# Kernel tuning notes

Hardware: AMD Instinct MI355X
Metric: run time of the kernel (lower is better)

## Reference

```python
import jax, jax.numpy as jnp
import numpy as np

V = 27578   # super-model vertex count (self.shape)
NJ = 24     # joints
NB = 10     # shape PCA coeffs
NP = (NJ - 1) * 9  # 207 pose-blend features
K = 24000   # kept vertices (to_keep)
B = 32
# standard SMPL kinematic tree: PARENTS[i] is the parent joint of joint i (i>=1)
PARENTS = np.array([0, 0, 0, 0, 1, 2, 3, 4, 5, 6, 7, 8, 9, 9, 9, 12, 13, 14, 16, 17, 18, 19, 20, 21], dtype=np.int32)


def setup_inputs() -> dict:
    key = jax.random.key(0)
    ks = jax.random.split(key, 8)
    pose = jax.random.normal(ks[0], (B, NJ, 3), dtype=jnp.float32) * 0.4
    betas = jax.random.normal(ks[1], (B, NB + 1), dtype=jnp.float32)  # last entry = gender flag
    J_regressor = jax.random.uniform(ks[2], (2, NJ, V), dtype=jnp.float32)
    J_regressor = J_regressor / jnp.sum(J_regressor, axis=-1, keepdims=True)
    v_template = jax.random.normal(ks[3], (2, V, 3), dtype=jnp.float32)
    shapedirs = jax.random.normal(ks[4], (2, V, 3, NB), dtype=jnp.float32) * 0.03
    posedirs = jax.random.normal(ks[5], (2, V, 3, NP), dtype=jnp.float32) * 0.01
    weights_all = jax.random.uniform(ks[6], (2, V, NJ), dtype=jnp.float32)
    weights_all = weights_all / jnp.sum(weights_all, axis=-1, keepdims=True)
    to_keep = jnp.sort(jax.random.randint(ks[7], (K,), 0, V, dtype=jnp.int32))
    return {"pose": pose, "betas": betas, "J_regressor": J_regressor,
            "v_template": v_template, "shapedirs": shapedirs, "posedirs": posedirs,
            "weights_all": weights_all, "to_keep": to_keep}


def rodrigues(r):
    """Axis-angle [N,3] -> rotation matrices [N,3,3] (Rodrigues formula)."""
    eps = jnp.float32(np.finfo(np.float32).eps)
    theta = jnp.maximum(jnp.linalg.norm(r, axis=-1, keepdims=True), eps)  # [N,1]
    rh = r / theta
    z = jnp.zeros_like(rh[:, 0])
    m = jnp.stack([z, -rh[:, 2], rh[:, 1],
                   rh[:, 2], z, -rh[:, 0],
                   -rh[:, 1], rh[:, 0], z], axis=1).reshape(-1, 3, 3)
    t = theta[:, :, None]  # [N,1,1]
    I = jnp.eye(3, dtype=r.dtype)
    return I + m * jnp.sin(t) + jnp.matmul(m, m) * (1.0 - jnp.cos(t))


def reference(pose, betas, J_regressor, v_template, shapedirs, posedirs, weights_all, to_keep):
    b = betas.shape[0]
    dt = pose.dtype
    g = betas[:, -1] > 0.5  # gender: True -> male (index 1)
    sel = lambda f, m: jnp.where(g[:, None, None], m, f)

    # shape blendshapes for both genders, select per sample
    vs_f = jnp.einsum('bs,vcs->bvc', betas[:, :NB], shapedirs[0]) + v_template[0]
    vs_m = jnp.einsum('bs,vcs->bvc', betas[:, :NB], shapedirs[1]) + v_template[1]

    J_f = jnp.einsum('jv,bvc->bjc', J_regressor[0], vs_f)
    J_m = jnp.einsum('jv,bvc->bjc', J_regressor[1], vs_m)
    J = sel(J_f, J_m)  # [b,24,3]

    # Rodrigues per joint
    R = rodrigues(pose.reshape(-1, 3)).reshape(b, NJ, 3, 3)

    # pose blendshapes
    lrot = (R[:, 1:] - jnp.eye(3, dtype=dt)).reshape(b, NP)  # [b,207]
    off_f = jnp.einsum('bp,vcp->bvc', lrot, posedirs[0])
    off_m = jnp.einsum('bp,vcp->bvc', lrot, posedirs[1])
    v_posed = sel(vs_f, vs_m) + sel(off_f, off_m)  # [b,V,3]

    # local joint transforms [b,24,4,4]
    J_rel = jnp.concatenate([J[:, :1], J[:, 1:] - J[:, PARENTS[1:]]], axis=1)
    A = jnp.concatenate([R, J_rel[..., None]], axis=-1)  # [b,24,3,4]
    bottom = jnp.broadcast_to(jnp.array([0., 0., 0., 1.], dtype=dt), (b, NJ, 1, 4))
    A = jnp.concatenate([A, bottom], axis=2)

    # kinematic chain (sequential 24-joint tree)
    Gs = [A[:, 0]]
    for i in range(1, NJ):
        Gs.append(jnp.matmul(Gs[int(PARENTS[i])], A[:, i]))
    G = jnp.stack(Gs, axis=1)  # [b,24,4,4]

    # subtract rest-pose joint contribution: results = G - pack(G @ [J;0])
    Jh0 = jnp.concatenate([J, jnp.zeros((b, NJ, 1), dtype=dt)], axis=-1)
    corr = jnp.einsum('bjpq,bjq->bjp', G, Jh0)
    results = G.at[:, :, :, 3].add(-corr)

    Jh1 = jnp.concatenate([J, jnp.ones((b, NJ, 1), dtype=dt)], axis=-1)
    joints = jnp.einsum('bjpq,bjq->bjp', results, Jh1)[:, :, :3]

    # linear blend skinning with gender-matched weights
    w = jnp.where(g[:, None, None], weights_all[1][None], weights_all[0][None])  # [b,V,24]
    T = jnp.einsum('bjpq,bvj->bvpq', results, w)  # [b,V,4,4]
    vh = jnp.concatenate([v_posed, jnp.ones((b, V, 1), dtype=dt)], axis=-1)
    v = jnp.einsum('bvpq,bvq->bvp', T, vh)[:, :, :3]

    root = joints[:, :1]
    result = (v - root)[:, to_keep, :]  # [b,K,3]
    return result
```

## Files before the change

### kernel.cpp

```cpp
#include <hip/hip_runtime.h>
#include <hip/hip_bf16.h>
#include <cstdint>
#include <cstddef>

#define V      27578
#define NJ     24
#define KK     24000
#define NT2    1724
#define NCHUNK 21
#define VCHUNK 1314

#define LPD    0
#define LA     12288
#define LRB    16000
#define LVP    24192
#define LT     26368
#define LWA    36608
#define LTM2   37120
#define LROOT2 37216
#define LPERM2 37312
#define LCNT2  37344
#define LKB    37348
#define LDSW   37364

#define WS_JS   0
#define WS_LA   33264
#define WS_RB   36976
#define WS_ROOT 45168
#define WS_PERM 45264
#define WS_CNT  45296
#define WS_KB   45300

typedef short short8 __attribute__((ext_vector_type(8)));
typedef float f32x4 __attribute__((ext_vector_type(4)));
typedef float f32x4a __attribute__((ext_vector_type(4), aligned(4)));

union S8U4 { unsigned u[4]; uint4 u4; short8 s; };

__device__ __forceinline__ unsigned pk2(float a, float b) {
    __hip_bfloat162 h = __float22bfloat162_rn(float2{a, b});
    union { __hip_bfloat162 h; unsigned u; } cv; cv.h = h;
    return cv.u;
}

#define BAR_LGKM() do { \
    asm volatile("s_waitcnt lgkmcnt(0)\n\ts_barrier" ::: "memory"); \
    __builtin_amdgcn_sched_barrier(0); \
} while (0)

__constant__ int d_par[24] = {0,0,0,0,1,2,3,4,5,6,7,8,9,9,9,12,13,14,16,17,18,19,20,21};

__global__ __launch_bounds__(256) void k_js(const float* __restrict__ jreg,
                                            const float* __restrict__ vtmpl,
                                            const float* __restrict__ sdirs,
                                            float* __restrict__ ws) {
    const int chunk = blockIdx.x, jg = blockIdx.y, g = blockIdx.z;
    const int tid = threadIdx.x;
    float acc[4][33];
#pragma unroll
    for (int a = 0; a < 4; ++a)
#pragma unroll
        for (int o = 0; o < 33; ++o) acc[a][o] = 0.f;

    const int v0 = chunk * VCHUNK;
    const int v1 = (v0 + VCHUNK < V) ? v0 + VCHUNK : V;
    const float* jr0 = jreg + (size_t)g * NJ * V;
    const float* sd  = sdirs + (size_t)g * V * 30;
    const float* tm  = vtmpl + (size_t)g * V * 3;

    for (int v = v0 + tid; v < v1; v += 256) {
        float jv[4];
#pragma unroll
        for (int a = 0; a < 4; ++a) jv[a] = jr0[(size_t)(jg*4 + a) * V + v];
        float b[33];
        const float* sdv = sd + (size_t)v * 30;
#pragma unroll
        for (int o = 0; o < 30; o += 2) {
            float2 q = *(const float2*)(sdv + o);
            b[o] = q.x; b[o+1] = q.y;
        }
        b[30] = tm[(size_t)v*3 + 0];
        b[31] = tm[(size_t)v*3 + 1];
        b[32] = tm[(size_t)v*3 + 2];
#pragma unroll
        for (int a = 0; a < 4; ++a)
#pragma unroll
            for (int o = 0; o < 33; ++o) acc[a][o] += jv[a] * b[o];
    }

#pragma unroll
    for (int a = 0; a < 4; ++a)
#pragma unroll
        for (int o = 0; o < 33; ++o) {
            float x = acc[a][o];
#pragma unroll
            for (int s = 32; s >= 1; s >>= 1) x += __shfl_xor(x, s, 64);
            acc[a][o] = x;
        }

    __shared__ float red[4][132];
    const int wvi = tid >> 6, ln = tid & 63;
    if (ln == 0) {
#pragma unroll
        for (int a = 0; a < 4; ++a)
#pragma unroll
            for (int o = 0; o < 33; ++o) red[wvi][a*33 + o] = acc[a][o];
    }
    __syncthreads();
    if (tid < 132) {
        float s = red[0][tid] + red[1][tid] + red[2][tid] + red[3][tid];
        int a = tid / 33, o = tid % 33;
        int j = jg * 4 + a;
        ws[(size_t)((g*NJ + j)*33 + o) * NCHUNK + chunk] = s;
    }
}

__global__ __launch_bounds__(256) void k_joint(const float* __restrict__ pose,
                                               const float* __restrict__ betas,
                                               const int*   __restrict__ to_keep,
                                               float* __restrict__ ws) {
    const int bid = (int)blockIdx.x;
    const int t = threadIdx.x;
    int* wsI = (int*)ws;
    unsigned* wsU = (unsigned*)ws;

    if (bid >= 32) {
        int idx = (bid - 32) * 256 + t;
        if (idx <= NT2) {
            int target = idx * 16;
            int lo = 0, hi = KK;
            while (lo < hi) { int m = (lo + hi) >> 1; if (to_keep[m] < target) lo = m + 1; else hi = m; }
            wsI[WS_KB + idx] = lo;
        }
        return;
    }

    __shared__ float gflag[32];
    __shared__ int   permJ[33];
    __shared__ float jsJ[792];
    __shared__ float Jloc[96];
    __shared__ float AJ[288];
    __shared__ float GS[288];

    if (t < 32) gflag[t] = betas[t*11 + 10];
    __syncthreads();
    if (t < 32) {
        bool male = gflag[t] > 0.5f;
        unsigned gm = (unsigned)__ballot(male);
        int cnt0 = 32 - __popc(gm);
        unsigned below = (1u << t) - 1u;
        int slot = male ? (cnt0 + __popc(gm & below)) : __popc((~gm) & below);
        permJ[slot] = t;
        if (t == 0) permJ[32] = cnt0;
    }
    __syncthreads();

    const int slot = bid;
    const int b = permJ[slot];
    const int gi = (gflag[b] > 0.5f) ? 1 : 0;

    if (bid == 0) {
        if (t < 32) wsI[WS_PERM + t] = permJ[t];
        if (t == 0) wsI[WS_CNT] = permJ[32];
    }

    for (int o = t; o < 792; o += 256) {
        const float* p = ws + WS_JS + (size_t)(gi*792 + o) * NCHUNK;
        float s = 0.f;
#pragma unroll
        for (int c = 0; c < NCHUNK; ++c) s += p[c];
        jsJ[o] = s;
    }
    __syncthreads();

    if (t < 72) {
        int j = t / 3, c = t - 3*j;
        const float* jsb = jsJ + j*33;
        float s = jsb[30 + c];
#pragma unroll
        for (int q = 0; q < 10; ++q) s += jsb[c*10 + q] * betas[b*11 + q];
        Jloc[j*4 + c] = s;
    }
    __syncthreads();

    if (t < 24) {
        const float* pp = pose + (size_t)(b*24 + t) * 3;
        float rx = pp[0], ry = pp[1], rz = pp[2];
        float th = fmaxf(sqrtf(rx*rx + ry*ry + rz*rz), 1.1920929e-07f);
        float inv = 1.0f / th;
        float ux = rx*inv, uy = ry*inv, uz = rz*inv;
        float st = sinf(th), ct = cosf(th), oc = 1.0f - ct;
        float* A = AJ + t*12;
        A[0] = ct + oc*ux*ux;    A[1] = oc*ux*uy - st*uz; A[2]  = oc*ux*uz + st*uy;
        A[4] = oc*ux*uy + st*uz; A[5] = ct + oc*uy*uy;    A[6]  = oc*uy*uz - st*ux;
        A[8] = oc*ux*uz - st*uy; A[9] = oc*uy*uz + st*ux; A[10] = ct + oc*uz*uz;
        int par = d_par[t];
#pragma unroll
        for (int r = 0; r < 3; ++r)
            A[r*4 + 3] = Jloc[t*4 + r] - (t > 0 ? Jloc[par*4 + r] : 0.f);
    }
    __syncthreads();

    if (t < 116) {
        float f[2];
#pragma unroll
        for (int h = 0; h < 2; ++h) {
            int k = 2*t + h;
            float val = 0.f;
            if (k < 207) {
                int j = k / 9 + 1, rc = k - 9*(j-1);
                int r = rc / 3, c = rc - 3*r;
                val = AJ[j*12 + r*4 + c] - (r == c ? 1.f : 0.f);
            } else if (k >= 208 && k < 218) {
                val = betas[b*11 + (k - 208)];
            }
            f[h] = val;
        }
        wsU[WS_LA + slot*116 + t] = pk2(f[0], f[1]);
    }

    if (t < 12) {
        constexpr int kPar[24] = {0,0,0,0,1,2,3,4,5,6,7,8,9,9,9,12,13,14,16,17,18,19,20,21};
        const int r = t >> 2, c = t & 3;
        float Greg[24];
        Greg[0] = AJ[t];
#pragma unroll
        for (int j = 1; j < 24; ++j) {
            const int par = kPar[j];
            float a0 = AJ[j*12 + 0 + c];
            float a1 = AJ[j*12 + 4 + c];
            float a2 = AJ[j*12 + 8 + c];
            float g0 = __shfl(Greg[par], r*4 + 0, 64);
            float g1 = __shfl(Greg[par], r*4 + 1, 64);
            float g2 = __shfl(Greg[par], r*4 + 2, 64);
            float g3 = __shfl(Greg[par], r*4 + 3, 64);
            Greg[j] = g0*a0 + g1*a1 + g2*a2 + (c == 3 ? g3 : 0.f);
        }
#pragma unroll
        for (int j = 0; j < 24; ++j) {
            float t0 = __shfl(Greg[j], r*4 + 0, 64);
            float t1 = __shfl(Greg[j], r*4 + 1, 64);
            float t2 = __shfl(Greg[j], r*4 + 2, 64);
            float corr = t0*Jloc[j*4 + 0] + t1*Jloc[j*4 + 1] + t2*Jloc[j*4 + 2];
            if (c == 3) Greg[j] -= corr;
            GS[j*12 + t] = Greg[j];
        }
    }
    __syncthreads();

    {
        int kg = t >> 6, rem = t & 63, n = rem >> 2, wq = rem & 3;
        int j0 = kg*8 + 2*wq;
        float f0 = (j0 < 24 && n < 12) ? GS[j0*12 + n] : 0.f;
        float f1 = (j0 + 1 < 24 && n < 12) ? GS[(j0+1)*12 + n] : 0.f;
        wsU[WS_RB + slot*256 + t] = pk2(f0, f1);
    }
    if (t < 3) {
        float s = GS[t*4 + 3];
#pragma unroll
        for (int q = 0; q < 3; ++q) s += GS[t*4 + q] * Jloc[q];
        ws[WS_ROOT + slot*3 + t] = s;
    }
}

__global__ __launch_bounds__(1024)
__attribute__((amdgpu_waves_per_eu(4, 4)))
void k_pose(const float* __restrict__ posedirs,
            const float* __restrict__ sdirs,
            const float* __restrict__ vtmpl,
            const float* __restrict__ wall,
            const int*   __restrict__ to_keep,
            const float* __restrict__ ws,
            float* __restrict__ out) {
    extern __shared__ float L[];
    unsigned* Lu = (unsigned*)L;
    int* Li = (int*)L;
    const unsigned* wsU = (const unsigned*)ws;
    const int* wsI = (const int*)ws;
    const int t = threadIdx.x;
    const int l = t & 63, wv = t >> 6;
    const int lm = l & 15, lg = l >> 4;
    const int bid = (int)blockIdx.x;

    int pdoff[5], pdladr[5];
    bool pdok[5], pdq3[5];
#pragma unroll
    for (int n = 0; n < 5; ++n) {
        int e = t + 1024*n;
        bool ok = e < 4992;
        pdok[n] = ok;
        int e2 = ok ? e : 0;
        int row = e2 / 52, k4 = (e2 - 52*row) * 4;
        int g = row / 48, rr = row - 48*g;
        pdoff[n] = g*(V*621) + rr*207 + k4;
        int kw = k4 >> 1;
        pdladr[n] = LPD + row*128 + (kw ^ ((row & 7) << 2));
        pdq3[n] = (k4 == 204);
    }
    int sdoff = 0, sdladr = 0;
    if (t < 480) {
        int w = 2*t;
        int g = w / 480, w2 = w - 480*g;
        int row = w2 / 10, j = (w2 - 10*row) >> 1;
        int rowg = g*48 + row;
        sdoff = g*(V*30) + w2;
        sdladr = LPD + rowg*128 + ((104 + j) ^ ((rowg & 7) << 2));
    }
    int tmoff = 0;
    if (t < 48)  { int w = 2*t; int g = w/48;  tmoff = g*(V*3) + (w - 48*g); }
    int woff = 0, wladr = 0;
    if (t < 384) {
        int g = t/192, i = t - 192*g;
        int v = i/12, wi = i - 12*v;
        int kgrp = wi >> 2, wq = wi & 3;
        int j0 = kgrp*8 + 2*wq;
        woff = g*(V*24) + v*24 + j0;
        wladr = LWA + g*256 + kgrp*64 + v*4 + wq;
    }

    float4 pdreg[5]; float2 sdreg = {0,0}, tmreg = {0,0}, wreg = {0,0};

    const int PDLIM = 2*V*621 - 4;
    const int SDLIM = 2*V*30 - 2;
    const int TMLIM = 2*V*3 - 2;
    const int WLIM  = 2*V*24 - 2;

    auto issue_loads = [&](int itm) {
        const int vb = itm * 16;
#pragma unroll
        for (int n = 0; n < 5; ++n) {
            int a = vb*621 + pdoff[n];
            if (a > PDLIM) a = PDLIM;
            f32x4a q = *(const f32x4a*)(posedirs + a);
            pdreg[n].x = q.x;
            pdreg[n].y = q.y;
            pdreg[n].z = q.z;
            pdreg[n].w = pdq3[n] ? 0.f : q.w;
        }
        if (t < 480) { int a = vb*30 + sdoff; if (a > SDLIM) a = SDLIM; sdreg = *(const float2*)(sdirs + a); }
        if (t < 48)  { int a = vb*3  + tmoff; if (a > TMLIM) a = TMLIM; tmreg = *(const float2*)(vtmpl + a); }
        if (t < 384) { int a = vb*24 + woff;  if (a > WLIM)  a = WLIM;  wreg  = *(const float2*)(wall  + a); }
    };

    auto write_stage = [&]() {
#pragma unroll
        for (int n = 0; n < 5; ++n)
            if (pdok[n]) {
                uint2 v;
                v.x = pk2(pdreg[n].x, pdreg[n].y);
                v.y = pk2(pdreg[n].z, pdreg[n].w);
                *(uint2*)&Lu[pdladr[n]] = v;
            }
        if (t < 480) Lu[sdladr] = pk2(sdreg.x, sdreg.y);
        if (t < 48)  { L[LTM2 + 2*t] = tmreg.x; L[LTM2 + 2*t + 1] = tmreg.y; }
        if (t < 384) Lu[wladr] = pk2(wreg.x, wreg.y);
    };

    issue_loads(bid);

    {
        for (int i = t; i < 928; i += 1024)
            *(uint4*)&Lu[LA + 4*i] = *(const uint4*)&wsU[WS_LA + 4*i];
        for (int i = t; i < 2048; i += 1024)
            *(uint4*)&Lu[LRB + 4*i] = *(const uint4*)&wsU[WS_RB + 4*i];
        if (t < 96)  L[LROOT2 + t] = ws[WS_ROOT + t];
        if (t < 32)  Li[LPERM2 + t] = wsI[WS_PERM + t];
        if (t == 0)  Li[LCNT2] = wsI[WS_CNT];
        if (t < 8) {
            int idx = bid + 256*t;
            int kst = KK, ken = KK;
            if (idx < NT2) { kst = wsI[WS_KB + idx]; ken = wsI[WS_KB + idx + 1]; }
            Li[LKB + t] = kst; Li[LKB + 8 + t] = ken;
        }
        if (t < 128) Lu[LWA + (t >> 6)*256 + 192 + (t & 63)] = 0;
        if (t < 288) {
            int row = t / 3, j2 = 109 + (t - 3*(t/3));
            Lu[LPD + row*128 + (j2 ^ ((row & 7) << 2))] = 0;
        }
        __syncthreads();
    }

    const int cnt0v = Li[LCNT2];
    const int cnt1 = 32 - cnt0v;
    const int m0 = (cnt0v + 15) >> 4, m1 = (cnt1 + 15) >> 4;
    const int ntA = 3*m0, ntasks = 3*(m0 + m1);

    int rb0 = -1, nt0 = 0, sb0 = 0, ct0 = 0, gi0 = 0;
    if (wv < ntasks) {
        int gi = (wv >= ntA) ? 1 : 0; int tt = gi ? wv - ntA : wv;
        int mt = tt / 3; nt0 = tt - 3*mt;
        sb0 = gi ? cnt0v : 0; ct0 = gi ? cnt1 : cnt0v;
        rb0 = sb0 + mt*16; gi0 = gi;
    }

    const int bs = t >> 5, kl0 = t & 31;
    const int borig = Li[LPERM2 + bs];
    const float rt0 = L[LROOT2 + bs*3 + 0];
    const float rt1 = L[LROOT2 + bs*3 + 1];
    const float rt2 = L[LROOT2 + bs*3 + 2];
    const int s4 = (lm & 7) << 2;

    write_stage();
    __syncthreads();

    int li = 0;
    for (int item = bid; item < NT2; item += 256, ++li) {
        const bool more = (item + 256 < NT2);
        if (more) issue_loads(item + 256);

        f32x4 acc0 = {0,0,0,0};
        if (rb0 >= 0) {
            const unsigned* ap = Lu + LA + (rb0 + lm)*116 + (lg << 2);
            const unsigned* bp = Lu + LPD + (gi0*48 + nt0*16 + lm)*128;
#pragma unroll
            for (int kk = 0; kk < 7; ++kk) {
                S8U4 a; a.u4 = *(const uint4*)(ap + kk*16);
                S8U4 bb; bb.u4 = *(const uint4*)(bp + ((kk*16 + (lg << 2)) ^ s4));
                acc0 = __builtin_amdgcn_mfma_f32_16x16x32_bf16(a.s, bb.s, acc0, 0, 0, 0);
            }
        }

        if (rb0 >= 0) {
            int n = nt0*16 + lm;
            int vd = n / 3, cd = n - 3*vd;
            float tmv = L[LTM2 + gi0*48 + n];
#pragma unroll
            for (int r = 0; r < 4; ++r) {
                int slot = rb0 + (lg << 2) + r;
                if ((unsigned)(slot - sb0) < (unsigned)ct0)
                    L[LVP + slot*68 + vd*4 + cd] = acc0[r] + tmv;
            }
        }

#pragma unroll
        for (int q = 0; q < 2; ++q) {
            int s = wv*2 + q;
            int gsl = (s >= cnt0v) ? 1 : 0;
            S8U4 a; a.u4 = *(const uint4*)(Lu + LWA + gsl*256 + lg*64 + lm*4);
            S8U4 b; b.u4 = *(const uint4*)(Lu + LRB + s*256 + lg*64 + lm*4);
            f32x4 acT = {0,0,0,0};
            acT = __builtin_amdgcn_mfma_f32_16x16x32_bf16(a.s, b.s, acT, 0, 0, 0);
#pragma unroll
            for (int r = 0; r < 4; ++r)
                L[LT + s*320 + (lg*4 + r)*20 + lm] = acT[r];
        }
        BAR_LGKM();

        const int kst = Li[LKB + li], ken = Li[LKB + 8 + li];
        const int v0w = item * 16;
        for (int k = kst + kl0; k < ken; k += 32) {
            const int vr = to_keep[k] - v0w;
            const float4 vp = *(const float4*)&L[LVP + bs*68 + vr*4];
            const float4 t0 = *(const float4*)&L[LT + bs*320 + vr*20];
            const float4 t1 = *(const float4*)&L[LT + bs*320 + vr*20 + 4];
            const float4 t2 = *(const float4*)&L[LT + bs*320 + vr*20 + 8];
            const size_t ob = ((size_t)borig*KK + (size_t)k)*3;
            out[ob]   = t0.x*vp.x + t0.y*vp.y + t0.z*vp.z + t0.w - rt0;
            out[ob+1] = t1.x*vp.x + t1.y*vp.y + t1.z*vp.z + t1.w - rt1;
            out[ob+2] = t2.x*vp.x + t2.y*vp.y + t2.z*vp.z + t2.w - rt2;
        }
        if (more) write_stage();
        BAR_LGKM();
    }
}

extern "C" void kernel_launch(void* const* d_in, const int* in_sizes, int n_in,
                              void* d_out, int out_size, void* d_ws, size_t ws_size,
                              hipStream_t stream) {
    const float* pose     = (const float*)d_in[0];
    const float* betas    = (const float*)d_in[1];
    const float* jreg     = (const float*)d_in[2];
    const float* vtmpl    = (const float*)d_in[3];
    const float* sdirs    = (const float*)d_in[4];
    const float* posedirs = (const float*)d_in[5];
    const float* wall     = (const float*)d_in[6];
    const int*   to_keep  = (const int*)d_in[7];
    float* ws  = (float*)d_ws;
    float* out = (float*)d_out;

    hipFuncSetAttribute((const void*)k_pose,
                        hipFuncAttributeMaxDynamicSharedMemorySize,
                        LDSW * 4);

    hipLaunchKernelGGL(k_js,    dim3(NCHUNK, 6, 2), dim3(256), 0, stream, jreg, vtmpl, sdirs, ws);
    hipLaunchKernelGGL(k_joint, dim3(40),           dim3(256), 0, stream, pose, betas, to_keep, ws);
    hipLaunchKernelGGL(k_pose,  dim3(256),          dim3(1024), LDSW * 4, stream,
                       posedirs, sdirs, vtmpl, wall, to_keep, ws, out);
}
```

Baseline: 67.25 us.

## Fuse three kernels into one cooperative kernel with grid syncs

Merges the joint-regression reduction, the per-batch kinematic chain, and the pose/skinning kernel into a single cooperative launch separated by two grid-wide syncs. The main pose kernel's first global prefetch is issued before the first grid sync, so it overlaps with the reduction and joint stages. This removes two kernel launch gaps, but adds grid-sync cost and drops the waves_per_eu attribute. All 256 blocks of 1024 threads must be co-resident for the cooperative launch to succeed.

```diff
diff --git a/kernel.cpp b/kernel.cpp
--- a/kernel.cpp
+++ b/kernel.cpp
@@ -1,7 +1,10 @@
 #include <hip/hip_runtime.h>
 #include <hip/hip_bf16.h>
+#include <hip/hip_cooperative_groups.h>
 #include <cstdint>
 #include <cstddef>
+
+namespace cg = cooperative_groups;
 
 #define V      27578
 #define NJ     24
@@ -23,6 +26,13 @@
 #define LKB    37348
 #define LDSW   37364
 
+#define PB_GF   0
+#define PB_PERM 32
+#define PB_JS   80
+#define PB_JL   880
+#define PB_AJ   980
+#define PB_GS   1280
+
 #define WS_JS   0
 #define WS_LA   33264
 #define WS_RB   36976
@@ -50,238 +60,92 @@
 
 __constant__ int d_par[24] = {0,0,0,0,1,2,3,4,5,6,7,8,9,9,9,12,13,14,16,17,18,19,20,21};
 
-__global__ __launch_bounds__(256) void k_js(const float* __restrict__ jreg,
-                                            const float* __restrict__ vtmpl,
-                                            const float* __restrict__ sdirs,
-                                            float* __restrict__ ws) {
-    const int chunk = blockIdx.x, jg = blockIdx.y, g = blockIdx.z;
-    const int tid = threadIdx.x;
-    float acc[4][33];
-#pragma unroll
-    for (int a = 0; a < 4; ++a)
-#pragma unroll
-        for (int o = 0; o < 33; ++o) acc[a][o] = 0.f;
-
-    const int v0 = chunk * VCHUNK;
-    const int v1 = (v0 + VCHUNK < V) ? v0 + VCHUNK : V;
-    const float* jr0 = jreg + (size_t)g * NJ * V;
-    const float* sd  = sdirs + (size_t)g * V * 30;
-    const float* tm  = vtmpl + (size_t)g * V * 3;
-
-    for (int v = v0 + tid; v < v1; v += 256) {
-        float jv[4];
-#pragma unroll
-        for (int a = 0; a < 4; ++a) jv[a] = jr0[(size_t)(jg*4 + a) * V + v];
-        float b[33];
-        const float* sdv = sd + (size_t)v * 30;
-#pragma unroll
-        for (int o = 0; o < 30; o += 2) {
-            float2 q = *(const float2*)(sdv + o);
-            b[o] = q.x; b[o+1] = q.y;
-        }
-        b[30] = tm[(size_t)v*3 + 0];
-        b[31] = tm[(size_t)v*3 + 1];
-        b[32] = tm[(size_t)v*3 + 2];
-#pragma unroll
-        for (int a = 0; a < 4; ++a)
-#pragma unroll
-            for (int o = 0; o < 33; ++o) acc[a][o] += jv[a] * b[o];
-    }
-
-#pragma unroll
-    for (int a = 0; a < 4; ++a)
-#pragma unroll
-        for (int o = 0; o < 33; ++o) {
-            float x = acc[a][o];
-#pragma unroll
-            for (int s = 32; s >= 1; s >>= 1) x += __shfl_xor(x, s, 64);
-            acc[a][o] = x;
-        }
-
-    __shared__ float red[4][132];
-    const int wvi = tid >> 6, ln = tid & 63;
-    if (ln == 0) {
-#pragma unroll
-        for (int a = 0; a < 4; ++a)
-#pragma unroll
-            for (int o = 0; o < 33; ++o) red[wvi][a*33 + o] = acc[a][o];
-    }
-    __syncthreads();
-    if (tid < 132) {
-        float s = red[0][tid] + red[1][tid] + red[2][tid] + red[3][tid];
-        int a = tid / 33, o = tid % 33;
-        int j = jg * 4 + a;
-        ws[(size_t)((g*NJ + j)*33 + o) * NCHUNK + chunk] = s;
-    }
-}
-
-__global__ __launch_bounds__(256) void k_joint(const float* __restrict__ pose,
-                                               const float* __restrict__ betas,
-                                               const int*   __restrict__ to_keep,
-                                               float* __restrict__ ws) {
-    const int bid = (int)blockIdx.x;
-    const int t = threadIdx.x;
-    int* wsI = (int*)ws;
-    unsigned* wsU = (unsigned*)ws;
-
-    if (bid >= 32) {
-        int idx = (bid - 32) * 256 + t;
-        if (idx <= NT2) {
-            int target = idx * 16;
-            int lo = 0, hi = KK;
-            while (lo < hi) { int m = (lo + hi) >> 1; if (to_keep[m] < target) lo = m + 1; else hi = m; }
-            wsI[WS_KB + idx] = lo;
-        }
-        return;
-    }
-
-    __shared__ float gflag[32];
-    __shared__ int   permJ[33];
-    __shared__ float jsJ[792];
-    __shared__ float Jloc[96];
-    __shared__ float AJ[288];
-    __shared__ float GS[288];
-
-    if (t < 32) gflag[t] = betas[t*11 + 10];
-    __syncthreads();
-    if (t < 32) {
-        bool male = gflag[t] > 0.5f;
-        unsigned gm = (unsigned)__ballot(male);
-        int cnt0 = 32 - __popc(gm);
-        unsigned below = (1u << t) - 1u;
-        int slot = male ? (cnt0 + __popc(gm & below)) : __popc((~gm) & below);
-        permJ[slot] = t;
-        if (t == 0) permJ[32] = cnt0;
-    }
-    __syncthreads();
-
-    const int slot = bid;
-    const int b = permJ[slot];
-    const int gi = (gflag[b] > 0.5f) ? 1 : 0;
-
-    if (bid == 0) {
-        if (t < 32) wsI[WS_PERM + t] = permJ[t];
-        if (t == 0) wsI[WS_CNT] = permJ[32];
-    }
-
-    for (int o = t; o < 792; o += 256) {
-        const float* p = ws + WS_JS + (size_t)(gi*792 + o) * NCHUNK;
-        float s = 0.f;
-#pragma unroll
-        for (int c = 0; c < NCHUNK; ++c) s += p[c];
-        jsJ[o] = s;
-    }
-    __syncthreads();
-
-    if (t < 72) {
-        int j = t / 3, c = t - 3*j;
-        const float* jsb = jsJ + j*33;
-        float s = jsb[30 + c];
-#pragma unroll
-        for (int q = 0; q < 10; ++q) s += jsb[c*10 + q] * betas[b*11 + q];
-        Jloc[j*4 + c] = s;
-    }
-    __syncthreads();
-
-    if (t < 24) {
-        const float* pp = pose + (size_t)(b*24 + t) * 3;
-        float rx = pp[0], ry = pp[1], rz = pp[2];
-        float th = fmaxf(sqrtf(rx*rx + ry*ry + rz*rz), 1.1920929e-07f);
-        float inv = 1.0f / th;
-        float ux = rx*inv, uy = ry*inv, uz = rz*inv;
-        float st = sinf(th), ct = cosf(th), oc = 1.0f - ct;
-        float* A = AJ + t*12;
-        A[0] = ct + oc*ux*ux;    A[1] = oc*ux*uy - st*uz; A[2]  = oc*ux*uz + st*uy;
-        A[4] = oc*ux*uy + st*uz; A[5] = ct + oc*uy*uy;    A[6]  = oc*uy*uz - st*ux;
-        A[8] = oc*ux*uz - st*uy; A[9] = oc*uy*uz + st*ux; A[10] = ct + oc*uz*uz;
-        int par = d_par[t];
-#pragma unroll
-        for (int r = 0; r < 3; ++r)
-            A[r*4 + 3] = Jloc[t*4 + r] - (t > 0 ? Jloc[par*4 + r] : 0.f);
-    }
-    __syncthreads();
-
-    if (t < 116) {
-        float f[2];
-#pragma unroll
-        for (int h = 0; h < 2; ++h) {
-            int k = 2*t + h;
-            float val = 0.f;
-            if (k < 207) {
-                int j = k / 9 + 1, rc = k - 9*(j-1);
-                int r = rc / 3, c = rc - 3*r;
-                val = AJ[j*12 + r*4 + c] - (r == c ? 1.f : 0.f);
-            } else if (k >= 208 && k < 218) {
-                val = betas[b*11 + (k - 208)];
-            }
-            f[h] = val;
-        }
-        wsU[WS_LA + slot*116 + t] = pk2(f[0], f[1]);
-    }
-
-    if (t < 12) {
-        constexpr int kPar[24] = {0,0,0,0,1,2,3,4,5,6,7,8,9,9,9,12,13,14,16,17,18,19,20,21};
-        const int r = t >> 2, c = t & 3;
-        float Greg[24];
-        Greg[0] = AJ[t];
-#pragma unroll
-        for (int j = 1; j < 24; ++j) {
-            const int par = kPar[j];
-            float a0 = AJ[j*12 + 0 + c];
-            float a1 = AJ[j*12 + 4 + c];
-            float a2 = AJ[j*12 + 8 + c];
-            float g0 = __shfl(Greg[par], r*4 + 0, 64);
-            float g1 = __shfl(Greg[par], r*4 + 1, 64);
-            float g2 = __shfl(Greg[par], r*4 + 2, 64);
-            float g3 = __shfl(Greg[par], r*4 + 3, 64);
-            Greg[j] = g0*a0 + g1*a1 + g2*a2 + (c == 3 ? g3 : 0.f);
-        }
-#pragma unroll
-        for (int j = 0; j < 24; ++j) {
-            float t0 = __shfl(Greg[j], r*4 + 0, 64);
-            float t1 = __shfl(Greg[j], r*4 + 1, 64);
-            float t2 = __shfl(Greg[j], r*4 + 2, 64);
-            float corr = t0*Jloc[j*4 + 0] + t1*Jloc[j*4 + 1] + t2*Jloc[j*4 + 2];
-            if (c == 3) Greg[j] -= corr;
-            GS[j*12 + t] = Greg[j];
-        }
-    }
-    __syncthreads();
-
-    {
-        int kg = t >> 6, rem = t & 63, n = rem >> 2, wq = rem & 3;
-        int j0 = kg*8 + 2*wq;
-        float f0 = (j0 < 24 && n < 12) ? GS[j0*12 + n] : 0.f;
-        float f1 = (j0 + 1 < 24 && n < 12) ? GS[(j0+1)*12 + n] : 0.f;
-        wsU[WS_RB + slot*256 + t] = pk2(f0, f1);
-    }
-    if (t < 3) {
-        float s = GS[t*4 + 3];
-#pragma unroll
-        for (int q = 0; q < 3; ++q) s += GS[t*4 + q] * Jloc[q];
-        ws[WS_ROOT + slot*3 + t] = s;
-    }
-}
-
 __global__ __launch_bounds__(1024)
-__attribute__((amdgpu_waves_per_eu(4, 4)))
-void k_pose(const float* __restrict__ posedirs,
-            const float* __restrict__ sdirs,
-            const float* __restrict__ vtmpl,
-            const float* __restrict__ wall,
-            const int*   __restrict__ to_keep,
-            const float* __restrict__ ws,
-            float* __restrict__ out) {
+void k_all(const float* __restrict__ jreg,
+           const float* __restrict__ vtmpl,
+           const float* __restrict__ sdirs,
+           const float* __restrict__ posedirs,
+           const float* __restrict__ wall,
+           const int*   __restrict__ to_keep,
+           const float* __restrict__ pose,
+           const float* __restrict__ betas,
+           float* __restrict__ ws,
+           float* __restrict__ out) {
     extern __shared__ float L[];
     unsigned* Lu = (unsigned*)L;
     int* Li = (int*)L;
-    const unsigned* wsU = (const unsigned*)ws;
-    const int* wsI = (const int*)ws;
+    unsigned* wsU = (unsigned*)ws;
+    int* wsI = (int*)ws;
     const int t = threadIdx.x;
+    const int bid = (int)blockIdx.x;
+    cg::grid_group grid = cg::this_grid();
+
+    if (bid < 252) {
+        const int chunk = bid % NCHUNK;
+        const int rem = bid / NCHUNK;
+        const int jg = rem % 6;
+        const int g  = rem / 6;
+        const int q  = t >> 8;
+        const int i  = t & 255;
+        const int o0 = (q == 0) ? 0 : (1 + 8*q);
+        const int sz = (q == 0) ? 9 : 8;
+        float acc[4][9];
+#pragma unroll
+        for (int a = 0; a < 4; ++a)
+#pragma unroll
+            for (int oi = 0; oi < 9; ++oi) acc[a][oi] = 0.f;
+        const int v0 = chunk * VCHUNK;
+        const int v1 = (v0 + VCHUNK < V) ? v0 + VCHUNK : V;
+        const float* jr0 = jreg + (size_t)g * NJ * V;
+        const float* sd  = sdirs + (size_t)g * V * 30;
+        const float* tm  = vtmpl + (size_t)g * V * 3;
+        for (int v = v0 + i; v < v1; v += 256) {
+            float jv[4];
+#pragma unroll
+            for (int a = 0; a < 4; ++a) jv[a] = jr0[(size_t)(jg*4 + a) * V + v];
+            float b[9];
+#pragma unroll
+            for (int oi = 0; oi < 9; ++oi) {
+                int o = o0 + oi;
+                float val = 0.f;
+                if (oi < sz) val = (o < 30) ? sd[(size_t)v*30 + o] : tm[(size_t)v*3 + (o - 30)];
+                b[oi] = val;
+            }
+#pragma unroll
+            for (int a = 0; a < 4; ++a)
+#pragma unroll
+                for (int oi = 0; oi < 9; ++oi) acc[a][oi] += jv[a] * b[oi];
+        }
+#pragma unroll
+        for (int a = 0; a < 4; ++a)
+#pragma unroll
+            for (int oi = 0; oi < 9; ++oi) {
+                float x = acc[a][oi];
+#pragma unroll
+                for (int s = 32; s >= 1; s >>= 1) x += __shfl_xor(x, s, 64);
+                acc[a][oi] = x;
+            }
+        const int wvA = t >> 6, lnA = t & 63;
+        if (lnA == 0) {
+#pragma unroll
+            for (int a = 0; a < 4; ++a)
+#pragma unroll
+                for (int oi = 0; oi < 9; ++oi)
+                    if (oi < sz) L[wvA*132 + a*33 + o0 + oi] = acc[a][oi];
+        }
+        __syncthreads();
+        if (t < 132) {
+            int a = t / 33, o = t % 33;
+            int oq = (o < 9) ? 0 : (o < 17) ? 1 : (o < 25) ? 2 : 3;
+            float s = L[(oq*4+0)*132 + a*33 + o] + L[(oq*4+1)*132 + a*33 + o]
+                    + L[(oq*4+2)*132 + a*33 + o] + L[(oq*4+3)*132 + a*33 + o];
+            int j = jg*4 + a;
+            ws[(size_t)((g*NJ + j)*33 + o) * NCHUNK + chunk] = s;
+        }
+    }
+
     const int l = t & 63, wv = t >> 6;
     const int lm = l & 15, lg = l >> 4;
-    const int bid = (int)blockIdx.x;
-
     int pdoff[5], pdladr[5];
     bool pdok[5], pdq3[5];
 #pragma unroll
@@ -319,7 +183,6 @@
     }
 
     float4 pdreg[5]; float2 sdreg = {0,0}, tmreg = {0,0}, wreg = {0,0};
-
     const int PDLIM = 2*V*621 - 4;
     const int SDLIM = 2*V*30 - 2;
     const int TMLIM = 2*V*3 - 2;
@@ -357,6 +220,140 @@
     };
 
     issue_loads(bid);
+
+    grid.sync();
+
+    if (bid < 32) {
+        if (t < 32) L[PB_GF + t] = betas[t*11 + 10];
+        __syncthreads();
+        if (t < 32) {
+            bool male = L[PB_GF + t] > 0.5f;
+            unsigned gm = (unsigned)__ballot(male);
+            int cnt0 = 32 - __popc(gm);
+            unsigned below = (1u << t) - 1u;
+            int slot = male ? (cnt0 + __popc(gm & below)) : __popc((~gm) & below);
+            Li[PB_PERM + slot] = t;
+            if (t == 0) Li[PB_PERM + 32] = cnt0;
+        }
+        __syncthreads();
+
+        const int slot = bid;
+        const int b = Li[PB_PERM + slot];
+        const int gi = (L[PB_GF + b] > 0.5f) ? 1 : 0;
+
+        if (bid == 0) {
+            if (t < 32) wsI[WS_PERM + t] = Li[PB_PERM + t];
+            if (t == 0) wsI[WS_CNT] = Li[PB_PERM + 32];
+        }
+
+        if (t < 792) {
+            const float* p = ws + WS_JS + (size_t)(gi*792 + t) * NCHUNK;
+            float s = 0.f;
+#pragma unroll
+            for (int c = 0; c < NCHUNK; ++c) s += p[c];
+            L[PB_JS + t] = s;
+        }
+        __syncthreads();
+
+        if (t < 72) {
+            int j = t / 3, c = t - 3*j;
+            const float* jsb = L + PB_JS + j*33;
+            float s = jsb[30 + c];
+#pragma unroll
+            for (int q = 0; q < 10; ++q) s += jsb[c*10 + q] * betas[b*11 + q];
+            L[PB_JL + j*4 + c] = s;
+        }
+        __syncthreads();
+
+        if (t < 24) {
+            const float* pp = pose + (size_t)(b*24 + t) * 3;
+            float rx = pp[0], ry = pp[1], rz = pp[2];
+            float th = fmaxf(sqrtf(rx*rx + ry*ry + rz*rz), 1.1920929e-07f);
+            float inv = 1.0f / th;
+            float ux = rx*inv, uy = ry*inv, uz = rz*inv;
+            float st = sinf(th), ct = cosf(th), oc = 1.0f - ct;
+            float* A = L + PB_AJ + t*12;
+            A[0] = ct + oc*ux*ux;    A[1] = oc*ux*uy - st*uz; A[2]  = oc*ux*uz + st*uy;
+            A[4] = oc*ux*uy + st*uz; A[5] = ct + oc*uy*uy;    A[6]  = oc*uy*uz - st*ux;
+            A[8] = oc*ux*uz - st*uy; A[9] = oc*uy*uz + st*ux; A[10] = ct + oc*uz*uz;
+            int par = d_par[t];
+#pragma unroll
+            for (int r = 0; r < 3; ++r)
+                A[r*4 + 3] = L[PB_JL + t*4 + r] - (t > 0 ? L[PB_JL + par*4 + r] : 0.f);
+        }
+        __syncthreads();
+
+        if (t < 116) {
+            float f[2];
+#pragma unroll
+            for (int h = 0; h < 2; ++h) {
+                int k = 2*t + h;
+                float val = 0.f;
+                if (k < 207) {
+                    int j = k / 9 + 1, rc = k - 9*(j-1);
+                    int r = rc / 3, c = rc - 3*r;
+                    val = L[PB_AJ + j*12 + r*4 + c] - (r == c ? 1.f : 0.f);
+                } else if (k >= 208 && k < 218) {
+                    val = betas[b*11 + (k - 208)];
+                }
+                f[h] = val;
+            }
+            wsU[WS_LA + slot*116 + t] = pk2(f[0], f[1]);
+        }
+
+        if (t < 12) {
+            constexpr int kPar[24] = {0,0,0,0,1,2,3,4,5,6,7,8,9,9,9,12,13,14,16,17,18,19,20,21};
+            const int r = t >> 2, c = t & 3;
+            float Greg[24];
+            Greg[0] = L[PB_AJ + t];
+#pragma unroll
+            for (int j = 1; j < 24; ++j) {
+                const int par = kPar[j];
+                float a0 = L[PB_AJ + j*12 + 0 + c];
+                float a1 = L[PB_AJ + j*12 + 4 + c];
+                float a2 = L[PB_AJ + j*12 + 8 + c];
+                float g0 = __shfl(Greg[par], r*4 + 0, 64);
+                float g1 = __shfl(Greg[par], r*4 + 1, 64);
+                float g2 = __shfl(Greg[par], r*4 + 2, 64);
+                float g3 = __shfl(Greg[par], r*4 + 3, 64);
+                Greg[j] = g0*a0 + g1*a1 + g2*a2 + (c == 3 ? g3 : 0.f);
+            }
+#pragma unroll
+            for (int j = 0; j < 24; ++j) {
+                float t0 = __shfl(Greg[j], r*4 + 0, 64);
+                float t1 = __shfl(Greg[j], r*4 + 1, 64);
+                float t2 = __shfl(Greg[j], r*4 + 2, 64);
+                float corr = t0*L[PB_JL + j*4 + 0] + t1*L[PB_JL + j*4 + 1] + t2*L[PB_JL + j*4 + 2];
+                if (c == 3) Greg[j] -= corr;
+                L[PB_GS + j*12 + t] = Greg[j];
+            }
+        }
+        __syncthreads();
+
+        if (t < 256) {
+            int kg = t >> 6, rem2 = t & 63, n = rem2 >> 2, wq = rem2 & 3;
+            int j0 = kg*8 + 2*wq;
+            float f0 = (j0 < 24 && n < 12) ? L[PB_GS + j0*12 + n] : 0.f;
+            float f1 = (j0 + 1 < 24 && n < 12) ? L[PB_GS + (j0+1)*12 + n] : 0.f;
+            wsU[WS_RB + slot*256 + t] = pk2(f0, f1);
+        }
+        if (t < 3) {
+            float s = L[PB_GS + t*4 + 3];
+#pragma unroll
+            for (int q = 0; q < 3; ++q) s += L[PB_GS + t*4 + q] * L[PB_JL + q];
+            ws[WS_ROOT + slot*3 + t] = s;
+        }
+    } else if (bid < 34) {
+        int idx = (bid - 32) * 1024 + t;
+        if (idx <= NT2) {
+            int target = idx * 16;
+            int lo = 0, hi = KK;
+            while (lo < hi) { int m = (lo + hi) >> 1; if (to_keep[m] < target) lo = m + 1; else hi = m; }
+            wsI[WS_KB + idx] = lo;
+        }
+    }
+
+    grid.sync();
 
     {
         for (int i = t; i < 928; i += 1024)
@@ -478,12 +475,13 @@
     float* ws  = (float*)d_ws;
     float* out = (float*)d_out;
 
-    hipFuncSetAttribute((const void*)k_pose,
+    hipFuncSetAttribute((const void*)k_all,
                         hipFuncAttributeMaxDynamicSharedMemorySize,
                         LDSW * 4);
 
-    hipLaunchKernelGGL(k_js,    dim3(NCHUNK, 6, 2), dim3(256), 0, stream, jreg, vtmpl, sdirs, ws);
-    hipLaunchKernelGGL(k_joint, dim3(40),           dim3(256), 0, stream, pose, betas, to_keep, ws);
-    hipLaunchKernelGGL(k_pose,  dim3(256),          dim3(1024), LDSW * 4, stream,
-                       posedirs, sdirs, vtmpl, wall, to_keep, ws, out);
+    void* args[] = {(void*)&jreg, (void*)&vtmpl, (void*)&sdirs, (void*)&posedirs,
+                    (void*)&wall, (void*)&to_keep, (void*)&pose, (void*)&betas,
+                    (void*)&ws, (void*)&out};
+    hipLaunchCooperativeKernel((const void*)k_all, dim3(256), dim3(1024),
+                               args, LDSW * 4, stream);
 }
```

Result: slower. 142.5 us (+111.9%).
